# Performance work log

Hardware: AMD Instinct MI355X
Metric: run time of the kernel (lower is better)

The kernel has to match this reference:

```python
import jax, jax.numpy as jnp
import numpy as np

B, H, W = 8, 512, 1024
SAMPLE_RATIO = 0.2
G = int(H * W * SAMPLE_RATIO)  # 104857 triplets per image
EPS = 1e-6
DELTA_COS = 0.867
DELTA_DIFF = 0.005  # filter_mask is called with hardcoded 0.005
DELTA_Z = 1e-5
SCALE = 1.0


def setup_inputs() -> dict:
    rng = np.random.default_rng(0)
    # positive depths in a realistic metric range
    target = rng.uniform(0.1, 10.0, size=(B, 1, H, W)).astype(np.float32)
    prediction = rng.uniform(0.1, 10.0, size=(B, 1, H, W)).astype(np.float32)
    mask = (rng.random((B, H, W)) > 0.05).astype(np.float32)
    # realistic pinhole intrinsics
    intrinsic = np.zeros((B, 3, 3), dtype=np.float32)
    intrinsic[:, 0, 0] = 1100.0 + rng.uniform(-50, 50, B)  # fx
    intrinsic[:, 1, 1] = 1100.0 + rng.uniform(-50, 50, B)  # fy
    intrinsic[:, 0, 2] = W / 2 + rng.uniform(-5, 5, B)     # u0
    intrinsic[:, 1, 2] = H / 2 + rng.uniform(-5, 5, B)     # v0
    intrinsic[:, 2, 2] = 1.0
    # without replacement (randperm-prefix semantics), pad with 0 if short
    ps = []
    for _ in range(3):
        pk = np.zeros((B, G), dtype=np.int32)
        for b in range(B):
            valid = np.flatnonzero(mask[b].ravel() > EPS)
            n = min(G, valid.size)
            pk[b, :n] = rng.choice(valid, size=n, replace=False)
        ps.append(pk)
    return {
        "prediction": jnp.asarray(prediction),
        "target": jnp.asarray(target),
        "mask": jnp.asarray(mask),
        "intrinsic": jnp.asarray(intrinsic),
        "p1": jnp.asarray(ps[0]),
        "p2": jnp.asarray(ps[1]),
        "p3": jnp.asarray(ps[2]),
    }


def _to_pw(depth, intrinsic):
    # depth: [B,H,W] -> pw: [B,H,W,3]
    f = intrinsic[:, 0, 0][:, None, None]
    u0 = intrinsic[:, 0, 2][:, None, None]
    v0 = intrinsic[:, 1, 2][:, None, None]
    u = jnp.arange(W, dtype=depth.dtype)[None, None, :] - u0  # [B,1,W]
    v = jnp.arange(H, dtype=depth.dtype)[None, :, None] - v0  # [B,H,1]
    x = u * depth / f
    y = v * depth / f
    return jnp.stack([x, y, depth], axis=-1)


def _gather_groups(pw, p1, p2, p3):
    # pw: [B,H,W,3] -> groups: [B,G,3coords,3points]
    pwf = pw.reshape(B, H * W, 3)
    g1 = jnp.take_along_axis(pwf, p1[:, :, None].astype(jnp.int32), axis=1)
    g2 = jnp.take_along_axis(pwf, p2[:, :, None].astype(jnp.int32), axis=1)
    g3 = jnp.take_along_axis(pwf, p3[:, :, None].astype(jnp.int32), axis=1)
    return jnp.stack([g1, g2, g3], axis=-1)


def _diffs(pts):
    # pts: [B,G,3c,3p] -> pw_diff: [B,G,3coords,3diffs] (12,13,23)
    return jnp.stack([pts[..., 1] - pts[..., 0],
                      pts[..., 2] - pts[..., 0],
                      pts[..., 2] - pts[..., 1]], axis=-1)


def _forward(prediction, target, mask, intrinsic, p1, p2, p3):
    pw_gt = _to_pw(target[:, 0], intrinsic)
    pw_pred = _to_pw(prediction[:, 0], intrinsic)

    gt_g = _gather_groups(pw_gt, p1, p2, p3)      # [B,G,3,3]
    pred_g = _gather_groups(pw_pred, p1, p2, p3)  # [B,G,3,3]

    # --- filter_mask on GT groups ---
    pw_diff = _diffs(gt_g)                                    # [B,G,3c,3d]
    energy = jnp.einsum("bgci,bgcj->bgij", pw_diff, pw_diff)  # gram of diffs
    qn = jnp.sqrt(jnp.sum(pw_diff * pw_diff, axis=2))         # [B,G,3d]
    nm = qn[..., :, None] * qn[..., None, :]
    norm_energy = energy / (nm + EPS)
    mask_cos = jnp.sum(jnp.abs(norm_energy) > DELTA_COS, axis=(2, 3)) > 3
    mask_pad = jnp.sum(gt_g[:, :, 2, :] > DELTA_Z, axis=2) == 3
    mask_x = jnp.sum(jnp.abs(pw_diff[:, :, 0, :]) < DELTA_DIFF, axis=2) > 0
    mask_y = jnp.sum(jnp.abs(pw_diff[:, :, 1, :]) < DELTA_DIFF, axis=2) > 0
    mask_z = jnp.sum(jnp.abs(pw_diff[:, :, 2, :]) < DELTA_DIFF, axis=2) > 0
    valid = mask_pad & ~((mask_x & mask_y & mask_z) | mask_cos)  # [B,G]

    # faithful replication of pw_groups_pred[pw_groups_pred[:,:,2,:]==0] = 1e-4
    # (bool mask over dims [B,G,3] indexes the coord axis, remaining axis is points)
    cond = pred_g[:, :, 2, :] == 0.0
    pred_g = jnp.where(cond[:, :, :, None], 1e-4, pred_g)

    # --- virtual normals ---
    def normal(pts):
        p12 = pts[..., 1] - pts[..., 0]  # [B,G,3]
        p13 = pts[..., 2] - pts[..., 0]
        n = jnp.cross(p12, p13, axis=-1)
        nn = jnp.linalg.norm(n, axis=-1, keepdims=True)
        nn = nn + (nn == 0.0).astype(n.dtype) * EPS
        return n / nn

    loss_g = jnp.sum(jnp.abs(normal(gt_g) - normal(pred_g)), axis=-1)  # [B,G]

    lf = loss_g.reshape(-1)
    vf = valid.reshape(-1)
    total = lf.shape[0]
    n = jnp.sum(vf.astype(jnp.int32))
    s = jnp.sort(jnp.where(vf, lf, -1e30))  # invalid sink to the front
    start = (total - n) + n // 4
    keep = jnp.arange(total) >= start
    denom = jnp.maximum(n - n // 4, 1).astype(lf.dtype)
    return jnp.sum(jnp.where(keep, s, 0.0)) / denom * SCALE


def reference(prediction, target, mask, intrinsic, p1, p2, p3):
    return _forward(prediction, target, mask, intrinsic, p1, p2, p3)
```

## Files before the change

### kernel.cpp

```cpp
#include <hip/hip_runtime.h>

#define B_ 8
#define H_ 512
#define W_ 1024
#define HW_ (H_ * W_)
#define G_ 104857
#define TILE_ 512
#define TILES_ ((G_ + TILE_ - 1) / TILE_)
#define NBLK_ (TILES_ * B_)
#define EPS_ 1e-6f
#define DCOS_ 0.867f
#define DDIFF_ 0.005f
#define DZ_ 1e-5f

#define NBIN_ 256
#define BINSCALE_ 73.0f

#define NRBLK_ 64
#define ROWS_PER_ ((NBLK_ + NRBLK_ - 1) / NRBLK_)

#define OFF_BHIST 0
#define OFF_BSUM  (NBLK_ * NBIN_ * 2)
#define OFF_GBINS (OFF_BSUM + NBLK_ * 4)
#define OFF_GSUM  (OFF_GBINS + NBIN_ * 4)
#define OFF_DONE  (OFF_GSUM + 8)

struct F3 { float x, y, z; };
__device__ __forceinline__ F3 f3sub(F3 a, F3 b) { return {a.x - b.x, a.y - b.y, a.z - b.z}; }
__device__ __forceinline__ float f3dot(F3 a, F3 b) { return a.x * b.x + a.y * b.y + a.z * b.z; }
__device__ __forceinline__ F3 f3cross(F3 a, F3 b) {
    return {a.y * b.z - a.z * b.y, a.z * b.x - a.x * b.z, a.x * b.y - a.y * b.x};
}

__global__ void __launch_bounds__(256)
compute_kernel(const float* __restrict__ pred, const float* __restrict__ targ,
               const float* __restrict__ intr,
               const int* __restrict__ p1, const int* __restrict__ p2,
               const int* __restrict__ p3,
               unsigned short* __restrict__ bhist, float* __restrict__ bsum,
               unsigned int* __restrict__ gbins, double* __restrict__ gsum,
               unsigned int* __restrict__ donecnt)
{
    __shared__ unsigned int hc[NBIN_];
    const int t = threadIdx.x;
    hc[t] = 0u;
    __syncthreads();

    const int img = blockIdx.x & 7;
    const int base = (blockIdx.x >> 3) * TILE_;

    const float fx = intr[img * 9 + 0];
    const float u0 = intr[img * 9 + 2];
    const float v0 = intr[img * 9 + 5];
    const float invf = 1.0f / fx;
    const float* tb = targ + (size_t)img * HW_;
    const float* pb = pred + (size_t)img * HW_;
    const int goff = img * G_;

    const int gA = base + t;
    const int gB = base + 256 + t;
    const bool inB = gB < G_;
    int a1 = p1[goff + gA], a2 = p2[goff + gA], a3 = p3[goff + gA];
    int b1 = inB ? p1[goff + gB] : 0;
    int b2 = inB ? p2[goff + gB] : 0;
    int b3 = inB ? p3[goff + gB] : 0;
    float tA1 = tb[a1], tA2 = tb[a2], tA3 = tb[a3];
    float pA1 = pb[a1], pA2 = pb[a2], pA3 = pb[a3];
    float tB1 = tb[b1], tB2 = tb[b2], tB3 = tb[b3];
    float pB1 = pb[b1], pB2 = pb[b2], pB3 = pb[b3];

    auto tri = [&](int i1, int i2, int i3, float dt1, float dt2, float dt3,
                   float dp1, float dp2, float dp3, float& loss) -> bool {
        auto mk = [&](int i, float d) -> F3 {
            float u = (float)(i & (W_ - 1));
            float v = (float)(i >> 10);
            return F3{(u - u0) * d * invf, (v - v0) * d * invf, d};
        };
        F3 G1 = mk(i1, dt1), G2 = mk(i2, dt2), G3 = mk(i3, dt3);
        F3 P1 = mk(i1, dp1), P2 = mk(i2, dp2), P3 = mk(i3, dp3);

        F3 d12 = f3sub(G2, G1), d13 = f3sub(G3, G1), d23 = f3sub(G3, G2);
        float e11 = f3dot(d12, d12), e22 = f3dot(d13, d13), e33 = f3dot(d23, d23);
        float e12 = f3dot(d12, d13), e13 = f3dot(d12, d23), e23 = f3dot(d13, d23);
        float q1 = sqrtf(e11), q2 = sqrtf(e22), q3 = sqrtf(e33);
        int cnt = 0;
        cnt += (e11 > DCOS_ * (q1 * q1 + EPS_)) ? 1 : 0;
        cnt += (e22 > DCOS_ * (q2 * q2 + EPS_)) ? 1 : 0;
        cnt += (e33 > DCOS_ * (q3 * q3 + EPS_)) ? 1 : 0;
        cnt += (fabsf(e12) > DCOS_ * (q1 * q2 + EPS_)) ? 2 : 0;
        cnt += (fabsf(e13) > DCOS_ * (q1 * q3 + EPS_)) ? 2 : 0;
        cnt += (fabsf(e23) > DCOS_ * (q2 * q3 + EPS_)) ? 2 : 0;
        bool mask_cos = cnt > 3;
        bool mask_pad = (G1.z > DZ_) && (G2.z > DZ_) && (G3.z > DZ_);
        bool mx = (fabsf(d12.x) < DDIFF_) || (fabsf(d13.x) < DDIFF_) || (fabsf(d23.x) < DDIFF_);
        bool my = (fabsf(d12.y) < DDIFF_) || (fabsf(d13.y) < DDIFF_) || (fabsf(d23.y) < DDIFF_);
        bool mz = (fabsf(d12.z) < DDIFF_) || (fabsf(d13.z) < DDIFF_) || (fabsf(d23.z) < DDIFF_);
        bool valid = mask_pad && !((mx && my && mz) || mask_cos);
        if (!valid) { loss = 0.0f; return false; }

        bool c0 = (P1.z == 0.0f), c1 = (P2.z == 0.0f), c2 = (P3.z == 0.0f);
        if (c0) { P1.x = 1e-4f; P2.x = 1e-4f; P3.x = 1e-4f; }
        if (c1) { P1.y = 1e-4f; P2.y = 1e-4f; P3.y = 1e-4f; }
        if (c2) { P1.z = 1e-4f; P2.z = 1e-4f; P3.z = 1e-4f; }

        auto vnormal = [](F3 A, F3 Bp, F3 C) -> F3 {
            F3 a = f3sub(Bp, A), c = f3sub(C, A);
            F3 n = f3cross(a, c);
            float d = f3dot(n, n);
            float r = (d > 0.0f) ? rsqrtf(d) : 0.0f;
            return F3{n.x * r, n.y * r, n.z * r};
        };
        F3 ng = vnormal(G1, G2, G3);
        F3 nd = vnormal(P1, P2, P3);
        loss = fabsf(ng.x - nd.x) + fabsf(ng.y - nd.y) + fabsf(ng.z - nd.z);
        return true;
    };

    float lA = 0.0f, lB = 0.0f;
    bool vA = tri(a1, a2, a3, tA1, tA2, tA3, pA1, pA2, pA3, lA);
    bool vB = inB && tri(b1, b2, b3, tB1, tB2, tB3, pB1, pB2, pB3, lB);

    if (vA) atomicAdd(&hc[min((int)(lA * BINSCALE_), NBIN_ - 1)], 1u);
    if (vB) atomicAdd(&hc[min((int)(lB * BINSCALE_), NBIN_ - 1)], 1u);

    float lsum = (vA ? lA : 0.0f) + (vB ? lB : 0.0f);
    for (int off = 32; off > 0; off >>= 1) lsum += __shfl_down(lsum, off, 64);
    __shared__ float wsum[4];
    if ((t & 63) == 0) wsum[t >> 6] = lsum;
    __syncthreads();
    if (t == 0) bsum[blockIdx.x] = wsum[0] + wsum[1] + wsum[2] + wsum[3];

    bhist[(size_t)blockIdx.x * NBIN_ + t] = (unsigned short)hc[t];

    if (blockIdx.x == 0) {
        gbins[t] = 0u;
        if (t == 0) { *gsum = 0.0; *donecnt = 0u; }
    }
}

__global__ void __launch_bounds__(256)
reduce_kernel(const unsigned short* __restrict__ bhist, const float* __restrict__ bsum,
              unsigned int* __restrict__ gbins, double* __restrict__ gsum,
              unsigned int* __restrict__ donecnt, float* __restrict__ out)
{
    const int t = threadIdx.x;
    const int r0 = blockIdx.x * ROWS_PER_;
    const int r1 = min(NBLK_, r0 + ROWS_PER_);
    unsigned int acc = 0;
    for (int r = r0; r < r1; ++r) acc += (unsigned int)bhist[(size_t)r * NBIN_ + t];
    if (acc) atomicAdd(&gbins[t], acc);

    if (blockIdx.x == 0) {
        double ls = 0.0;
        for (int i = t; i < NBLK_; i += 256) ls += (double)bsum[i];
        for (int off = 32; off > 0; off >>= 1) ls += __shfl_down(ls, off, 64);
        __shared__ double ws[4];
        if ((t & 63) == 0) ws[t >> 6] = ls;
        __syncthreads();
        if (t == 0) atomicAdd(gsum, ws[0] + ws[1] + ws[2] + ws[3]);
    }

    __shared__ unsigned int lastFlag;
    __syncthreads();
    if (t == 0) {
        __threadfence();
        lastFlag = (atomicAdd(donecnt, 1u) == (unsigned int)(NRBLK_ - 1)) ? 1u : 0u;
    }
    __syncthreads();
    if (!lastFlag) return;

    unsigned int myc = atomicAdd(&gbins[t], 0u);
    __shared__ unsigned int scc[256];
    scc[t] = myc;
    __syncthreads();
    for (int off = 1; off < 256; off <<= 1) {
        unsigned int ac = (t >= off) ? scc[t - off] : 0u;
        __syncthreads();
        scc[t] += ac;
        __syncthreads();
    }
    unsigned int tot = scc[255];
    if (tot == 0u) { if (t == 0) out[0] = 0.0f; return; }
    unsigned int r4 = tot / 4u;
    unsigned int K = tot - r4;
    unsigned int cprev = (t == 0) ? 0u : scc[t - 1];
    if (scc[t] > r4 && cprev <= r4) {
        double dropped = 0.0;
        for (int j = 0; j < t; ++j)
            dropped += (double)(scc[j] - (j == 0 ? 0u : scc[j - 1]))
                       * (((double)j + 0.5) / (double)BINSCALE_);
        dropped += (double)(r4 - cprev) * (((double)t + 0.5) / (double)BINSCALE_);
        double ts = atomicAdd(gsum, 0.0);
        out[0] = (float)((ts - dropped) / (double)K);
    }
}

extern "C" void kernel_launch(void* const* d_in, const int* in_sizes, int n_in,
                              void* d_out, int out_size, void* d_ws, size_t ws_size,
                              hipStream_t stream)
{
    const float* pred = (const float*)d_in[0];
    const float* targ = (const float*)d_in[1];
    const float* intr = (const float*)d_in[3];
    const int* p1 = (const int*)d_in[4];
    const int* p2 = (const int*)d_in[5];
    const int* p3 = (const int*)d_in[6];
    float* out = (float*)d_out;

    unsigned char* ws = (unsigned char*)d_ws;
    unsigned short* bhist = (unsigned short*)(ws + OFF_BHIST);
    float* bsum = (float*)(ws + OFF_BSUM);
    unsigned int* gbins = (unsigned int*)(ws + OFF_GBINS);
    double* gsum = (double*)(ws + OFF_GSUM);
    unsigned int* donecnt = (unsigned int*)(ws + OFF_DONE);

    compute_kernel<<<NBLK_, 256, 0, stream>>>(pred, targ, intr, p1, p2, p3,
                                              bhist, bsum, gbins, gsum, donecnt);
    reduce_kernel<<<NRBLK_, 256, 0, stream>>>(bhist, bsum, gbins, gsum, donecnt, out);
}
```

Before: 125.1 us.

## Interleave target/prediction into float2 buffer and process four triplets per thread

Adds a pre-pass kernel that interleaves target and prediction depths into a float2 array, so each random gather fetches both values in a single 8-byte load instead of two separate scattered loads. The compute kernel now uses 128-thread blocks, each thread handling four triplets with all index and depth loads issued up front to raise memory-level parallelism. The cost is an extra full read and write of 32 MB of depth data through the new kernel, plus a larger workspace footprint.

```diff
diff --git a/kernel.cpp b/kernel.cpp
--- a/kernel.cpp
+++ b/kernel.cpp
@@ -8,6 +8,7 @@
 #define TILE_ 512
 #define TILES_ ((G_ + TILE_ - 1) / TILE_)
 #define NBLK_ (TILES_ * B_)
+#define CBLK_ 128
 #define EPS_ 1e-6f
 #define DCOS_ 0.867f
 #define DDIFF_ 0.005f
@@ -24,6 +25,7 @@
 #define OFF_GBINS (OFF_BSUM + NBLK_ * 4)
 #define OFF_GSUM  (OFF_GBINS + NBIN_ * 4)
 #define OFF_DONE  (OFF_GSUM + 8)
+#define OFF_TP    (1 << 20)
 
 struct F3 { float x, y, z; };
 __device__ __forceinline__ F3 f3sub(F3 a, F3 b) { return {a.x - b.x, a.y - b.y, a.z - b.z}; }
@@ -33,8 +35,19 @@
 }
 
 __global__ void __launch_bounds__(256)
-compute_kernel(const float* __restrict__ pred, const float* __restrict__ targ,
-               const float* __restrict__ intr,
+interleave_kernel(const float* __restrict__ targ, const float* __restrict__ pred,
+                  float2* __restrict__ tp)
+{
+    const int q = blockIdx.x * 256 + threadIdx.x;
+    const float4 tq = ((const float4*)targ)[q];
+    const float4 pq = ((const float4*)pred)[q];
+    float4* o = (float4*)(tp + (size_t)q * 4);
+    o[0] = make_float4(tq.x, pq.x, tq.y, pq.y);
+    o[1] = make_float4(tq.z, pq.z, tq.w, pq.w);
+}
+
+__global__ void __launch_bounds__(128)
+compute_kernel(const float2* __restrict__ tp, const float* __restrict__ intr,
                const int* __restrict__ p1, const int* __restrict__ p2,
                const int* __restrict__ p3,
                unsigned short* __restrict__ bhist, float* __restrict__ bsum,
@@ -44,6 +57,7 @@
     __shared__ unsigned int hc[NBIN_];
     const int t = threadIdx.x;
     hc[t] = 0u;
+    hc[t + 128] = 0u;
     __syncthreads();
 
     const int img = blockIdx.x & 7;
@@ -53,31 +67,37 @@
     const float u0 = intr[img * 9 + 2];
     const float v0 = intr[img * 9 + 5];
     const float invf = 1.0f / fx;
-    const float* tb = targ + (size_t)img * HW_;
-    const float* pb = pred + (size_t)img * HW_;
+    const float2* tb = tp + (size_t)img * HW_;
     const int goff = img * G_;
 
-    const int gA = base + t;
-    const int gB = base + 256 + t;
-    const bool inB = gB < G_;
-    int a1 = p1[goff + gA], a2 = p2[goff + gA], a3 = p3[goff + gA];
-    int b1 = inB ? p1[goff + gB] : 0;
-    int b2 = inB ? p2[goff + gB] : 0;
-    int b3 = inB ? p3[goff + gB] : 0;
-    float tA1 = tb[a1], tA2 = tb[a2], tA3 = tb[a3];
-    float pA1 = pb[a1], pA2 = pb[a2], pA3 = pb[a3];
-    float tB1 = tb[b1], tB2 = tb[b2], tB3 = tb[b3];
-    float pB1 = pb[b1], pB2 = pb[b2], pB3 = pb[b3];
-
-    auto tri = [&](int i1, int i2, int i3, float dt1, float dt2, float dt3,
+    int i1[4], i2[4], i3[4];
+    bool inb[4];
+#pragma unroll
+    for (int j = 0; j < 4; ++j) {
+        const int g = base + j * CBLK_ + t;
+        inb[j] = g < G_;
+        const int gc = inb[j] ? g : 0;
+        i1[j] = p1[goff + gc];
+        i2[j] = p2[goff + gc];
+        i3[j] = p3[goff + gc];
+    }
+    float2 v1[4], v2[4], v3[4];
+#pragma unroll
+    for (int j = 0; j < 4; ++j) {
+        v1[j] = tb[i1[j]];
+        v2[j] = tb[i2[j]];
+        v3[j] = tb[i3[j]];
+    }
+
+    auto tri = [&](int i1_, int i2_, int i3_, float dt1, float dt2, float dt3,
                    float dp1, float dp2, float dp3, float& loss) -> bool {
         auto mk = [&](int i, float d) -> F3 {
             float u = (float)(i & (W_ - 1));
             float v = (float)(i >> 10);
             return F3{(u - u0) * d * invf, (v - v0) * d * invf, d};
         };
-        F3 G1 = mk(i1, dt1), G2 = mk(i2, dt2), G3 = mk(i3, dt3);
-        F3 P1 = mk(i1, dp1), P2 = mk(i2, dp2), P3 = mk(i3, dp3);
+        F3 G1 = mk(i1_, dt1), G2 = mk(i2_, dt2), G3 = mk(i3_, dt3);
+        F3 P1 = mk(i1_, dp1), P2 = mk(i2_, dp2), P3 = mk(i3_, dp3);
 
         F3 d12 = f3sub(G2, G1), d13 = f3sub(G3, G1), d23 = f3sub(G3, G2);
         float e11 = f3dot(d12, d12), e22 = f3dot(d13, d13), e33 = f3dot(d23, d23);
@@ -116,24 +136,31 @@
         return true;
     };
 
-    float lA = 0.0f, lB = 0.0f;
-    bool vA = tri(a1, a2, a3, tA1, tA2, tA3, pA1, pA2, pA3, lA);
-    bool vB = inB && tri(b1, b2, b3, tB1, tB2, tB3, pB1, pB2, pB3, lB);
-
-    if (vA) atomicAdd(&hc[min((int)(lA * BINSCALE_), NBIN_ - 1)], 1u);
-    if (vB) atomicAdd(&hc[min((int)(lB * BINSCALE_), NBIN_ - 1)], 1u);
-
-    float lsum = (vA ? lA : 0.0f) + (vB ? lB : 0.0f);
+    float lsum = 0.0f;
+#pragma unroll
+    for (int j = 0; j < 4; ++j) {
+        float l = 0.0f;
+        bool v = tri(i1[j], i2[j], i3[j], v1[j].x, v2[j].x, v3[j].x,
+                     v1[j].y, v2[j].y, v3[j].y, l);
+        v = v && inb[j];
+        if (v) {
+            atomicAdd(&hc[min((int)(l * BINSCALE_), NBIN_ - 1)], 1u);
+            lsum += l;
+        }
+    }
+
     for (int off = 32; off > 0; off >>= 1) lsum += __shfl_down(lsum, off, 64);
-    __shared__ float wsum[4];
+    __shared__ float wsum[2];
     if ((t & 63) == 0) wsum[t >> 6] = lsum;
     __syncthreads();
-    if (t == 0) bsum[blockIdx.x] = wsum[0] + wsum[1] + wsum[2] + wsum[3];
+    if (t == 0) bsum[blockIdx.x] = wsum[0] + wsum[1];
 
     bhist[(size_t)blockIdx.x * NBIN_ + t] = (unsigned short)hc[t];
+    bhist[(size_t)blockIdx.x * NBIN_ + t + 128] = (unsigned short)hc[t + 128];
 
     if (blockIdx.x == 0) {
         gbins[t] = 0u;
+        gbins[t + 128] = 0u;
         if (t == 0) { *gsum = 0.0; *donecnt = 0u; }
     }
 }
@@ -213,8 +240,10 @@
     unsigned int* gbins = (unsigned int*)(ws + OFF_GBINS);
     double* gsum = (double*)(ws + OFF_GSUM);
     unsigned int* donecnt = (unsigned int*)(ws + OFF_DONE);
-
-    compute_kernel<<<NBLK_, 256, 0, stream>>>(pred, targ, intr, p1, p2, p3,
-                                              bhist, bsum, gbins, gsum, donecnt);
+    float2* tp = (float2*)(ws + OFF_TP);
+
+    interleave_kernel<<<(B_ * HW_) / (4 * 256), 256, 0, stream>>>(targ, pred, tp);
+    compute_kernel<<<NBLK_, CBLK_, 0, stream>>>(tp, intr, p1, p2, p3,
+                                                bhist, bsum, gbins, gsum, donecnt);
     reduce_kernel<<<NRBLK_, 256, 0, stream>>>(bhist, bsum, gbins, gsum, donecnt, out);
 }
```

Measured after the change: 133.7 us. 6.9% more time.
